# Kernel optimization log

Hardware: AMD Instinct MI355X
Metric: run time of the kernel (lower is better)

Reference implementation:

```python
import jax, jax.numpy as jnp
import numpy as np

EMBED_DIM = 1024
NUM_HEADS = 16
SEQ = 2048
BATCH = 2


def setup_inputs() -> dict:
    key = jax.random.key(0)
    ks = jax.random.split(key, 9)
    E = EMBED_DIM
    gain = 1.0 / np.sqrt(2.0)  # xavier_uniform with gain 1/sqrt(2) (qkv_same_dim)
    limit = gain * np.sqrt(6.0 / (E + E))
    q = jax.random.normal(ks[0], (SEQ, BATCH, E), dtype=jnp.float32)
    k = jax.random.normal(ks[1], (SEQ, BATCH, E), dtype=jnp.float32)
    v = jax.random.normal(ks[2], (SEQ, BATCH, E), dtype=jnp.float32)
    Wq = jax.random.uniform(ks[3], (E, E), jnp.float32, -limit, limit)
    Wk = jax.random.uniform(ks[4], (E, E), jnp.float32, -limit, limit)
    Wv = jax.random.uniform(ks[5], (E, E), jnp.float32, -limit, limit)
    bq = jnp.zeros((E,), jnp.float32)
    bk = jnp.zeros((E,), jnp.float32)
    bv = jnp.zeros((E,), jnp.float32)
    return {"query": q, "key": k, "value": v,
            "Wq": Wq, "bq": bq, "Wk": Wk, "bk": bk, "Wv": Wv, "bv": bv}


def reference(query, key, value, Wq, bq, Wk, bk, Wv, bv):
    # Base Taylor attention path (norm_taylor=True, do_scale=True, has_out=False).
    L, B, E = query.shape
    H = NUM_HEADS
    hd = E // H
    scaling = E ** (-0.5)  # self.scaling = dim**-0.5, dim == embed_dim

    q = (query @ Wq + bq) * scaling          # (L, B, E)
    k = key @ Wk + bk                         # (S, B, E)
    v = value @ Wv + bv                       # (S, B, E)

    def split_heads(x):
        # (T, B, E) -> (B*H, T, hd)
        T = x.shape[0]
        return x.reshape(T, B * H, hd).transpose(1, 0, 2)

    qh, kh, vh = split_heads(q), split_heads(k), split_heads(v)

    # Taylor expansion of exp(qk) to first order: 1 + q.k
    attn = 1.0 + jnp.einsum('bld,bsd->bls', qh, kh)   # (B*H, L, S)
    attn = attn / attn.sum(axis=-1, keepdims=True)    # row-normalize
    out = jnp.einsum('bls,bsd->bld', attn, vh)        # (B*H, L, hd)
    out = out.transpose(1, 0, 2).reshape(L, B, E)     # (L, B, E)
    return out
```

## Files before the change

### kernel.cpp

```cpp
#include <hip/hip_runtime.h>
#include <hip/hip_bf16.h>

#define L_SEQ 2048
#define BATCH 2
#define ROWS 4096
#define E 1024
#define NH 16
#define HD 64

typedef __attribute__((ext_vector_type(4))) float f32x4;
typedef __attribute__((ext_vector_type(8))) __bf16 bf16x8;

#define SWZ(byt) ((byt) ^ ((((byt) >> 7) & 7) << 4))

__device__ __forceinline__ void gload16(const void* g, void* l) {
    __builtin_amdgcn_global_load_lds((const __attribute__((address_space(1))) void*)g,
                                     (__attribute__((address_space(3))) void*)l,
                                     16, 0, 0);
}

__global__ __launch_bounds__(256) void prep_w(const float* __restrict__ Wq,
                                              const float* __restrict__ Wk,
                                              const float* __restrict__ Wv,
                                              __bf16* __restrict__ Wt) {
    const int z = blockIdx.z;
    const float* W = (z == 0) ? Wq : ((z == 1) ? Wk : Wv);
    __bf16* dst = Wt + (size_t)z * E * E;
    __shared__ __align__(16) float t[64][65];
    const int n0 = blockIdx.x * 64, k0 = blockIdx.y * 64;
    const int r = threadIdx.x >> 2, c4 = threadIdx.x & 3;
#pragma unroll
    for (int j = 0; j < 4; ++j) {
        const float4 vv = *(const float4*)&W[(size_t)(k0 + r) * E + n0 + c4 * 16 + j * 4];
        t[r][c4 * 16 + j * 4 + 0] = vv.x;
        t[r][c4 * 16 + j * 4 + 1] = vv.y;
        t[r][c4 * 16 + j * 4 + 2] = vv.z;
        t[r][c4 * 16 + j * 4 + 3] = vv.w;
    }
    __syncthreads();
    bf16x8 o0, o1;
#pragma unroll
    for (int j = 0; j < 8; ++j) {
        o0[j] = (__bf16)t[c4 * 16 + j][r];
        o1[j] = (__bf16)t[c4 * 16 + 8 + j][r];
    }
    *(bf16x8*)&dst[(size_t)(n0 + r) * E + k0 + c4 * 16] = o0;
    *(bf16x8*)&dst[(size_t)(n0 + r) * E + k0 + c4 * 16 + 8] = o1;
}

__device__ __forceinline__ void stageB(const __bf16* __restrict__ gsrc, int row0, int kcol,
                                       char* ldsdst, int wv, int ln) {
#pragma unroll
    for (int r = 0; r < 4; ++r) {
        const int rowg = row0 + r * 32 + wv * 8 + (ln >> 3);
        const int c16 = (ln & 7) ^ (ln >> 3);
        gload16(gsrc + (size_t)rowg * E + kcol + c16 * 8,
                ldsdst + r * 4096 + wv * 1024);
    }
}

__device__ __forceinline__ void loadA_f32(const float* __restrict__ gsrc, int row0, int kcol,
                                          float4 (&o)[4][2], int wv, int ln) {
#pragma unroll
    for (int r = 0; r < 4; ++r) {
        const int rowg = row0 + r * 32 + wv * 8 + (ln >> 3);
        const int c16 = (ln & 7) ^ (ln >> 3);
        const float* p = gsrc + (size_t)rowg * E + kcol + c16 * 8;
        o[r][0] = *(const float4*)p;
        o[r][1] = *(const float4*)(p + 4);
    }
}

__device__ __forceinline__ void writeA_lds(const float4 (&a)[4][2], char* dst, int wv, int ln) {
#pragma unroll
    for (int r = 0; r < 4; ++r) {
        bf16x8 o;
        o[0] = (__bf16)a[r][0].x; o[1] = (__bf16)a[r][0].y;
        o[2] = (__bf16)a[r][0].z; o[3] = (__bf16)a[r][0].w;
        o[4] = (__bf16)a[r][1].x; o[5] = (__bf16)a[r][1].y;
        o[6] = (__bf16)a[r][1].z; o[7] = (__bf16)a[r][1].w;
        *(bf16x8*)(dst + r * 4096 + wv * 1024 + ln * 16) = o;
    }
}

__device__ __forceinline__ bf16x8 fragld(const char* base, int row, int kk, int kg) {
    return *(const bf16x8*)(base + row * 128 + ((((kk << 2) | kg) ^ (row & 7)) << 4));
}

#define PH_SYNC_BEGIN  __builtin_amdgcn_s_barrier(); \
                       asm volatile("s_waitcnt lgkmcnt(0)" ::: "memory"); \
                       __builtin_amdgcn_sched_barrier(0); \
                       __builtin_amdgcn_s_setprio(1);
#define PH_SYNC_END    __builtin_amdgcn_s_setprio(0); \
                       __builtin_amdgcn_s_barrier();

__global__ __launch_bounds__(256, 2) void gemm_qkv(const float* __restrict__ xq,
                                                   const float* __restrict__ xk,
                                                   const float* __restrict__ xv,
                                                   const __bf16* __restrict__ Wt,
                                                   const float* __restrict__ bq,
                                                   const float* __restrict__ bk,
                                                   const float* __restrict__ bv,
                                                   __bf16* __restrict__ Cb) {
    extern __shared__ __align__(16) char smem[];
    const int z = blockIdx.z;
    const float* A = (z == 0) ? xq : ((z == 1) ? xk : xv);
    const __bf16* B = Wt + (size_t)z * E * E;
    __bf16* C = Cb + (size_t)z * ROWS * E;
    const float* bias = (z == 0) ? bq : ((z == 1) ? bk : bv);
    const float alpha = (z == 0) ? 0.03125f : 1.0f;
    const int m0 = blockIdx.x * 128, n0 = blockIdx.y * 128;
    const int tid = threadIdx.x, ln = tid & 63, wv = tid >> 6;
    const int lr = ln & 15, kg = ln >> 4;
    const int wm = (wv & 1) * 64, wn = (wv >> 1) * 64;

    stageB(B, n0, 0,  smem + 32768, wv, ln);
    stageB(B, n0, 64, smem + 49152, wv, ln);
    float4 a0r[4][2], a1r[4][2];
    loadA_f32(A, m0, 0,  a0r, wv, ln);
    loadA_f32(A, m0, 64, a1r, wv, ln);
    asm volatile("s_waitcnt vmcnt(16)" ::: "memory");
    writeA_lds(a0r, smem,        wv, ln);
    writeA_lds(a1r, smem + 16384, wv, ln);
    asm volatile("s_waitcnt lgkmcnt(0)" ::: "memory");
    __builtin_amdgcn_s_barrier();

    f32x4 acc[4][4] = {};
    bf16x8 Af[4][2], Bf[2][2];
    float4 areg[4][2];

#define LOAD_B(nb) \
    _Pragma("unroll") for (int nn = 0; nn < 2; ++nn) \
    _Pragma("unroll") for (int kk = 0; kk < 2; ++kk) \
        Bf[nn][kk] = fragld(cB, wn + ((nb) + nn) * 16 + lr, kk, kg);
#define QUAD(q) \
    _Pragma("unroll") for (int m = 0; m < 4; ++m) \
    _Pragma("unroll") for (int nn = 0; nn < 2; ++nn) \
    _Pragma("unroll") for (int kk = 0; kk < 2; ++kk) \
        acc[m][2 * (q) + nn] = __builtin_amdgcn_mfma_f32_16x16x32_bf16(Af[m][kk], Bf[nn][kk], acc[m][2 * (q) + nn], 0, 0, 0);

    for (int T = 0; T < 16; ++T) {
        const char* cA = smem + (T & 1) * 16384;
        const char* cB = smem + 32768 + (T % 3) * 16384;
        char* nA = smem + (T & 1) * 16384;
        char* nB = smem + 32768 + ((T + 2) % 3) * 16384;
        if (T < 14) {
            loadA_f32(A, m0, (T + 2) * 64, areg, wv, ln);
            stageB(B, n0, (T + 2) * 64, nB, wv, ln);
        }
#pragma unroll
        for (int m = 0; m < 4; ++m)
#pragma unroll
            for (int kk = 0; kk < 2; ++kk)
                Af[m][kk] = fragld(cA, wm + m * 16 + lr, kk, kg);
        LOAD_B(0);
        PH_SYNC_BEGIN; QUAD(0); PH_SYNC_END;
        if (T < 14)       { asm volatile("s_waitcnt vmcnt(4)" ::: "memory"); }
        else if (T == 14) { asm volatile("s_waitcnt vmcnt(0)" ::: "memory"); }
        if (T < 14) writeA_lds(areg, nA, wv, ln);
        LOAD_B(2);
        PH_SYNC_BEGIN; QUAD(1); PH_SYNC_END;
    }
#undef LOAD_B
#undef QUAD

#pragma unroll
    for (int m = 0; m < 4; ++m) {
        const int rbase = m0 + wm + m * 16 + kg * 4;
#pragma unroll
        for (int n = 0; n < 4; ++n) {
            const int col = n0 + wn + n * 16 + lr;
            const float bcol = bias[col];
#pragma unroll
            for (int rr = 0; rr < 4; ++rr)
                C[(size_t)(rbase + rr) * E + col] = (__bf16)((acc[m][n][rr] + bcol) * alpha);
        }
    }
}

__global__ __launch_bounds__(256) void reduce_kv(const __bf16* __restrict__ Kb,
                                                 const __bf16* __restrict__ Vb,
                                                 float* __restrict__ Mpart,
                                                 float* __restrict__ ksumP,
                                                 float* __restrict__ vsumP) {
    const int bh = blockIdx.x, b = bh >> 4, h = bh & 15;
    const int ts = blockIdx.y;
    const int t0 = ts * 128;
    __shared__ __align__(16) __bf16 sK[128 * 64];
    __shared__ __align__(16) __bf16 sV[128 * 64];
    __shared__ float red_k[4][64];
    __shared__ float red_v[4][64];
    const int tid = threadIdx.x;
    const int lane = tid & 63, wave = tid >> 6;
    const int lr = lane & 15, kg = lane >> 4;

    float vk[8] = {}, vv[8] = {};
    const int d0 = (tid & 7) * 8;
#pragma unroll
    for (int i = 0; i < 4; ++i) {
        const int t = i * 32 + (tid >> 3);
        const size_t g = (size_t)((t0 + t) * 2 + b) * E + h * 64 + d0;
        const bf16x8 kv = *(const bf16x8*)&Kb[g];
        const bf16x8 vvv = *(const bf16x8*)&Vb[g];
        const int lo = (t * 128 + d0 * 2) ^ (wave << 5);
        *(bf16x8*)((char*)sK + lo) = kv;
        *(bf16x8*)((char*)sV + lo) = vvv;
#pragma unroll
        for (int j = 0; j < 8; ++j) { vk[j] += (float)kv[j]; vv[j] += (float)vvv[j]; }
    }
#pragma unroll
    for (int m = 8; m <= 32; m <<= 1)
#pragma unroll
        for (int j = 0; j < 8; ++j) {
            vk[j] += __shfl_xor(vk[j], m, 64);
            vv[j] += __shfl_xor(vv[j], m, 64);
        }
    if (lane < 8)
#pragma unroll
        for (int j = 0; j < 8; ++j) {
            red_k[wave][lane * 8 + j] = vk[j];
            red_v[wave][lane * 8 + j] = vv[j];
        }
    __syncthreads();

    f32x4 acc[4] = {};
#pragma unroll
    for (int kt = 0; kt < 4; ++kt) {
        const int tb = kt * 32;
        bf16x8 afr, bfr[4];
        const char* pv = (const char*)sV + (((tb + kg * 8) * 128 + (wave * 16 + lr) * 2) ^ (kg << 5));
#pragma unroll
        for (int j = 0; j < 8; ++j) afr[j] = *(const __bf16*)(pv + j * 128);
#pragma unroll
        for (int ni = 0; ni < 4; ++ni) {
            const char* pk = (const char*)sK + (((tb + kg * 8) * 128 + (ni * 16 + lr) * 2) ^ (kg << 5));
#pragma unroll
            for (int j = 0; j < 8; ++j) bfr[ni][j] = *(const __bf16*)(pk + j * 128);
        }
#pragma unroll
        for (int ni = 0; ni < 4; ++ni)
            acc[ni] = __builtin_amdgcn_mfma_f32_16x16x32_bf16(afr, bfr[ni], acc[ni], 0, 0, 0);
    }

    float* Mp = Mpart + ((size_t)bh * 16 + ts) * 4096;
#pragma unroll
    for (int ni = 0; ni < 4; ++ni)
#pragma unroll
        for (int rr = 0; rr < 4; ++rr)
            Mp[(wave * 16 + kg * 4 + rr) * 64 + ni * 16 + lr] = acc[ni][rr];
    if (tid < 64)
        ksumP[(bh * 16 + ts) * 64 + tid] = red_k[0][tid] + red_k[1][tid] + red_k[2][tid] + red_k[3][tid];
    else if (tid < 128) {
        const int d = tid - 64;
        vsumP[(bh * 16 + ts) * 64 + d] = red_v[0][d] + red_v[1][d] + red_v[2][d] + red_v[3][d];
    }
}

__global__ __launch_bounds__(256) void combine_m(const float* __restrict__ Mpart,
                                                 const float* __restrict__ ksumP,
                                                 const float* __restrict__ vsumP,
                                                 float* __restrict__ Mt,
                                                 float* __restrict__ ksum,
                                                 float* __restrict__ vsum) {
    const int blk = blockIdx.x, tid = threadIdx.x;
    if (blk < 256) {
        const int e2 = (blk * 256 + tid) * 2;
        const int bh = e2 >> 12, r = e2 & 4095;
        const float* src = Mpart + (size_t)bh * 16 * 4096 + r;
        float s0 = 0.f, s1 = 0.f;
#pragma unroll
        for (int ts = 0; ts < 16; ++ts) {
            s0 += src[ts * 4096];
            s1 += src[ts * 4096 + 1];
        }
        Mt[(size_t)bh * 4096 + r] = s0;
        Mt[(size_t)bh * 4096 + r + 1] = s1;
    } else if (blk < 264) {
        const int idx = (blk - 256) * 256 + tid;
        const int bh = idx >> 6, d = idx & 63;
        float s = 0.f;
#pragma unroll
        for (int ts = 0; ts < 16; ++ts) s += ksumP[bh * 1024 + ts * 64 + d];
        ksum[idx] = s;
    } else {
        const int idx = (blk - 264) * 256 + tid;
        const int bh = idx >> 6, d = idx & 63;
        float s = 0.f;
#pragma unroll
        for (int ts = 0; ts < 16; ++ts) s += vsumP[bh * 1024 + ts * 64 + d];
        vsum[idx] = s;
    }
}

__global__ __launch_bounds__(256) void taylor_out(const __bf16* __restrict__ Qb,
                                                  const float* __restrict__ Mt,
                                                  const float* __restrict__ ksum,
                                                  const float* __restrict__ vsum,
                                                  float* __restrict__ out) {
    const int b = blockIdx.y;
    const int lblk = blockIdx.x * 16;
    const int tid = threadIdx.x, lane = tid & 63, wave = tid >> 6;
    const int lr = lane & 15, kg = lane >> 4;
    __shared__ __align__(16) __bf16 sM[4][4096];
    for (int hh = 0; hh < 4; ++hh) {
        __syncthreads();
#pragma unroll
        for (int i = 0; i < 8; ++i) {
            const int idx = i * 256 + tid;
            const int hseg = idx >> 9, rem = idx & 511;
            const float* src = &Mt[(size_t)(b * 16 + hseg * 4 + hh) * 4096 + rem * 8];
            const float4 mA = *(const float4*)src;
            const float4 mB = *(const float4*)(src + 4);
            bf16x8 o;
            o[0] = (__bf16)mA.x; o[1] = (__bf16)mA.y; o[2] = (__bf16)mA.z; o[3] = (__bf16)mA.w;
            o[4] = (__bf16)mB.x; o[5] = (__bf16)mB.y; o[6] = (__bf16)mB.z; o[7] = (__bf16)mB.w;
            *(bf16x8*)((char*)&sM[hseg][0] + SWZ(rem * 16)) = o;
        }
        __syncthreads();
        const int h = wave * 4 + hh;
        const int bh = b * 16 + h;
        const int rA = (lblk + lr) * 2 + b;
        const bf16x8 a0 = *(const bf16x8*)&Qb[(size_t)rA * E + h * 64 + kg * 8];
        const bf16x8 a1 = *(const bf16x8*)&Qb[(size_t)rA * E + h * 64 + 32 + kg * 8];
        float p = 0.f;
        const float* ks = &ksum[bh * 64];
#pragma unroll
        for (int j = 0; j < 8; ++j)
            p += (float)a0[j] * ks[kg * 8 + j] + (float)a1[j] * ks[32 + kg * 8 + j];
        p += __shfl_xor(p, 16, 64);
        p += __shfl_xor(p, 32, 64);
        const float Z = 2048.0f + p;
        f32x4 acc[4] = {};
#pragma unroll
        for (int ni = 0; ni < 4; ++ni) {
            const int byt0 = (ni * 16 + lr) * 128 + kg * 16;
            const bf16x8 b0 = *(const bf16x8*)((const char*)&sM[wave][0] + SWZ(byt0));
            const bf16x8 b1 = *(const bf16x8*)((const char*)&sM[wave][0] + SWZ(byt0 + 64));
            acc[ni] = __builtin_amdgcn_mfma_f32_16x16x32_bf16(a0, b0, acc[ni], 0, 0, 0);
            acc[ni] = __builtin_amdgcn_mfma_f32_16x16x32_bf16(a1, b1, acc[ni], 0, 0, 0);
        }
        float invZ[4];
#pragma unroll
        for (int rr = 0; rr < 4; ++rr) invZ[rr] = 1.0f / __shfl(Z, kg * 4 + rr, 64);
        const float* vs = &vsum[bh * 64];
#pragma unroll
        for (int ni = 0; ni < 4; ++ni)
#pragma unroll
            for (int rr = 0; rr < 4; ++rr) {
                const int l_out = lblk + kg * 4 + rr;
                out[(size_t)(l_out * 2 + b) * E + h * 64 + ni * 16 + lr] =
                    (vs[ni * 16 + lr] + acc[ni][rr]) * invZ[rr];
            }
    }
}

extern "C" void kernel_launch(void* const* d_in, const int* in_sizes, int n_in,
                              void* d_out, int out_size, void* d_ws, size_t ws_size,
                              hipStream_t stream) {
    const float* q  = (const float*)d_in[0];
    const float* k  = (const float*)d_in[1];
    const float* v  = (const float*)d_in[2];
    const float* Wq = (const float*)d_in[3];
    const float* bq = (const float*)d_in[4];
    const float* Wk = (const float*)d_in[5];
    const float* bk = (const float*)d_in[6];
    const float* Wv = (const float*)d_in[7];
    const float* bv = (const float*)d_in[8];
    float* out = (float*)d_out;
    char* w = (char*)d_ws;
    __bf16* Wt = (__bf16*)(w);
    __bf16* Cb = (__bf16*)(w + 6291456);
    float* Mt    = (float*)(w + 31457280);
    float* ksum  = (float*)(w + 31981568);
    float* vsum  = (float*)(w + 31989760);
    float* Mpart = (float*)(w + 31997952);
    float* ksumP = (float*)(w + 40386560);
    float* vsumP = (float*)(w + 40517632);

    hipFuncSetAttribute((const void*)gemm_qkv,
                        hipFuncAttributeMaxDynamicSharedMemorySize, 81920);
    prep_w<<<dim3(16, 16, 3), 256, 0, stream>>>(Wq, Wk, Wv, Wt);
    gemm_qkv<<<dim3(32, 8, 3), 256, 81920, stream>>>(q, k, v, Wt, bq, bk, bv, Cb);
    reduce_kv<<<dim3(32, 16), 256, 0, stream>>>(Cb + (size_t)ROWS * E,
                                                Cb + 2 * (size_t)ROWS * E, Mpart, ksumP, vsumP);
    combine_m<<<272, 256, 0, stream>>>(Mpart, ksumP, vsumP, Mt, ksum, vsum);
    taylor_out<<<dim3(128, 2), 256, 0, stream>>>(Cb, Mt, ksum, vsum, out);
}
```

Measured before the change: 88.21 us.

## Deepen A-operand prefetch to three stages with double register buffers in QKV GEMM

The fp32 A tile for the QKV projection GEMM is now prefetched three K-steps ahead instead of two. Two alternating register buffers hold the in-flight loads, and the main loop is unrolled by two so the buffers swap roles each step. The vmcnt waits are retuned so more global loads stay outstanding while the MFMAs run, aiming to hide global-memory latency. The cost is higher register pressure from the second float4 buffer, which may reduce occupancy or cause spills.

Result: faster. 74.44 us (-15.6%).

```diff
diff --git a/kernel.cpp b/kernel.cpp
--- a/kernel.cpp
+++ b/kernel.cpp
@@ -114,20 +114,21 @@
     const int lr = ln & 15, kg = ln >> 4;
     const int wm = (wv & 1) * 64, wn = (wv >> 1) * 64;
 
+    float4 aregA[4][2], aregB[4][2];
+
     stageB(B, n0, 0,  smem + 32768, wv, ln);
     stageB(B, n0, 64, smem + 49152, wv, ln);
-    float4 a0r[4][2], a1r[4][2];
-    loadA_f32(A, m0, 0,  a0r, wv, ln);
-    loadA_f32(A, m0, 64, a1r, wv, ln);
-    asm volatile("s_waitcnt vmcnt(16)" ::: "memory");
-    writeA_lds(a0r, smem,        wv, ln);
-    writeA_lds(a1r, smem + 16384, wv, ln);
+    loadA_f32(A, m0, 0,  aregA, wv, ln);
+    loadA_f32(A, m0, 64, aregB, wv, ln);
+    asm volatile("s_waitcnt vmcnt(0)" ::: "memory");
+    writeA_lds(aregA, smem,        wv, ln);
+    writeA_lds(aregB, smem + 16384, wv, ln);
+    loadA_f32(A, m0, 128, aregA, wv, ln);
     asm volatile("s_waitcnt lgkmcnt(0)" ::: "memory");
     __builtin_amdgcn_s_barrier();
 
     f32x4 acc[4][4] = {};
     bf16x8 Af[4][2], Bf[2][2];
-    float4 areg[4][2];
 
 #define LOAD_B(nb) \
     _Pragma("unroll") for (int nn = 0; nn < 2; ++nn) \
@@ -139,28 +140,35 @@
     _Pragma("unroll") for (int kk = 0; kk < 2; ++kk) \
         acc[m][2 * (q) + nn] = __builtin_amdgcn_mfma_f32_16x16x32_bf16(Af[m][kk], Bf[nn][kk], acc[m][2 * (q) + nn], 0, 0, 0);
 
-    for (int T = 0; T < 16; ++T) {
-        const char* cA = smem + (T & 1) * 16384;
-        const char* cB = smem + 32768 + (T % 3) * 16384;
-        char* nA = smem + (T & 1) * 16384;
-        char* nB = smem + 32768 + ((T + 2) % 3) * 16384;
-        if (T < 14) {
-            loadA_f32(A, m0, (T + 2) * 64, areg, wv, ln);
-            stageB(B, n0, (T + 2) * 64, nB, wv, ln);
-        }
-#pragma unroll
-        for (int m = 0; m < 4; ++m)
-#pragma unroll
-            for (int kk = 0; kk < 2; ++kk)
-                Af[m][kk] = fragld(cA, wm + m * 16 + lr, kk, kg);
-        LOAD_B(0);
-        PH_SYNC_BEGIN; QUAD(0); PH_SYNC_END;
-        if (T < 14)       { asm volatile("s_waitcnt vmcnt(4)" ::: "memory"); }
-        else if (T == 14) { asm volatile("s_waitcnt vmcnt(0)" ::: "memory"); }
-        if (T < 14) writeA_lds(areg, nA, wv, ln);
-        LOAD_B(2);
-        PH_SYNC_BEGIN; QUAD(1); PH_SYNC_END;
-    }
+#define GBODY(TT, ALOAD, AWRITE)                                                  \
+    {                                                                             \
+        const int Tv = (TT);                                                      \
+        const char* cA = smem + (Tv & 1) * 16384;                                 \
+        const char* cB = smem + 32768 + (Tv % 3) * 16384;                         \
+        char* nA = smem + (Tv & 1) * 16384;                                       \
+        char* nB = smem + 32768 + ((Tv + 2) % 3) * 16384;                         \
+                                                           \
+        if (Tv <= 12) loadA_f32(A, m0, (Tv + 3) * 64, ALOAD, wv, ln);             \
+        if (Tv <= 13) stageB(B, n0, (Tv + 2) * 64, nB, wv, ln);                   \
+        _Pragma("unroll") for (int m = 0; m < 4; ++m)                             \
+        _Pragma("unroll") for (int kk = 0; kk < 2; ++kk)                          \
+            Af[m][kk] = fragld(cA, wm + m * 16 + lr, kk, kg);                     \
+        LOAD_B(0);                                                                \
+        PH_SYNC_BEGIN; QUAD(0); PH_SYNC_END;                                      \
+                                                           \
+        if (Tv <= 12)      { asm volatile("s_waitcnt vmcnt(12)" ::: "memory"); }  \
+        else if (Tv == 13) { asm volatile("s_waitcnt vmcnt(4)"  ::: "memory"); }  \
+        else if (Tv == 14) { asm volatile("s_waitcnt vmcnt(0)"  ::: "memory"); }  \
+        if (Tv <= 13) writeA_lds(AWRITE, nA, wv, ln);                             \
+        LOAD_B(2);                                                                \
+        PH_SYNC_BEGIN; QUAD(1); PH_SYNC_END;                                      \
+    }
+
+    for (int t = 0; t < 8; ++t) {
+        GBODY(2 * t,     aregB, aregA);
+        GBODY(2 * t + 1, aregA, aregB);
+    }
+#undef GBODY
 #undef LOAD_B
 #undef QUAD
 
```
